# Kernel optimization log

Hardware: AMD Instinct MI355X
Metric: run time of the kernel (lower is better)

## Reference

```python
import jax, jax.numpy as jnp
import numpy as np

BN_EPS = 1e-5
SQ_EPS = 1e-12


def _mlp(x, Wa, ba, g, b, Wb, bb):
    # Linear -> BatchNorm1d (eval mode, running mean=0 var=1) -> ReLU -> Linear
    h = x @ Wa + ba
    h = h * (g / jnp.sqrt(1.0 + BN_EPS)) + b
    h = jax.nn.relu(h)
    return h @ Wb + bb


def _signed_sqrt(x):
    # sqrt(relu(x)) - sqrt(relu(-x)); tiny eps keeps grads finite at exact zeros
    return jnp.sqrt(jax.nn.relu(x) + SQ_EPS) - jnp.sqrt(jax.nn.relu(-x) + SQ_EPS)


def setup_inputs() -> dict:
    G, NPG, H, POLY, L, T, TASKS, DEG = 1024, 16, 128, 16, 3, 1048576, 1, 8
    N = G * NPG
    P = G * NPG * NPG
    E = N * DEG
    key = jax.random.key(0)
    ks = iter(jax.random.split(key, 64))

    def nrm(shape, s):
        return jax.random.normal(next(ks), shape, jnp.float32) * s

    w = 0.06  # ~xavier scale for 128-dim layers
    inp = {
        'pair_x': nrm((P, POLY), 1.0),
        'diag_x': nrm((N, POLY), 1.0),
        'node_h': nrm((N, H), 1.0),
        'edge_h': nrm((E, H), 1.0),
        'W_pair': nrm((POLY, H), 0.12),
        'W_diag': nrm((POLY, H), 0.12),
        'Wd': nrm((2 * H, TASKS), w),
        'bd': jnp.zeros((TASKS,), jnp.float32),
    }
    for p, ind in (('m1', H), ('m2', H), ('up', 2 * H)):
        inp[p + '_Wa'] = nrm((L, ind, H), w)
        inp[p + '_ba'] = jnp.zeros((L, H), jnp.float32)
        inp[p + '_g'] = jnp.ones((L, H), jnp.float32)
        inp[p + '_b'] = jnp.zeros((L, H), jnp.float32)
        inp[p + '_Wb'] = nrm((L, H, H), w)
        inp[p + '_bb'] = jnp.zeros((L, H), jnp.float32)
    inp['edge_pos'] = jax.random.randint(next(ks), (E,), 0, P)
    n = jnp.arange(N)
    inp['diag_pos'] = (n // NPG) * NPG * NPG + (n % NPG) * NPG + (n % NPG)
    # graph-local triples: base pair block of the graph + random local pair ids
    tg = jax.random.randint(next(ks), (T,), 0, G) * (NPG * NPG)
    loc = jax.random.randint(next(ks), (3, T), 0, NPG * NPG)
    inp['triple_index'] = tg[None, :] + loc
    inp['batch'] = jnp.repeat(jnp.arange(G), NPG)
    inp['pair_x_batch'] = jnp.repeat(jnp.arange(G), NPG * NPG)
    inp['ptr'] = jnp.arange(G + 1) * NPG
    inp['pair_x_ptr'] = jnp.arange(G + 1) * (NPG * NPG)
    return inp


def reference(pair_x, diag_x, node_h, edge_h, W_pair, W_diag,
              m1_Wa, m1_ba, m1_g, m1_b, m1_Wb, m1_bb,
              m2_Wa, m2_ba, m2_g, m2_b, m2_Wb, m2_bb,
              up_Wa, up_ba, up_g, up_b, up_Wb, up_bb,
              Wd, bd,
              edge_pos, diag_pos, triple_index, batch, pair_x_batch, ptr, pair_x_ptr):
    P = pair_x.shape[0]
    # InitLayer: coalesce-add of pair, edge and diagonal (node) contributions
    pair_h = pair_x @ W_pair                             # [P, H]
    pair_h = pair_h.at[edge_pos].add(edge_h)
    pair_h = pair_h.at[diag_pos].add(node_h + diag_x @ W_diag)
    idx0, idx1, idx2 = triple_index[0], triple_index[1], triple_index[2]
    L = m1_Wa.shape[0]
    for l in range(L):  # fixed small layer count
        h1 = _mlp(pair_h, m1_Wa[l], m1_ba[l], m1_g[l], m1_b[l], m1_Wb[l], m1_bb[l])
        h2 = _mlp(pair_h, m2_Wa[l], m2_ba[l], m2_g[l], m2_b[l], m2_Wb[l], m2_bb[l])
        x3 = h1[idx1] * h2[idx2]                         # [T, H] gather-multiply
        agg = jax.ops.segment_sum(x3, idx0, num_segments=P)  # scatter_add
        agg = _signed_sqrt(agg)                          # use_sqrt=True
        h = jnp.concatenate([pair_h, agg], axis=-1)      # [P, 2H]
        pair_h = _mlp(h, up_Wa[l], up_ba[l], up_g[l], up_b[l], up_Wb[l], up_bb[l]) + pair_h
    G = ptr.shape[0] - 1
    agg_all = jax.ops.segment_sum(pair_h, pair_x_batch, num_segments=G)
    agg_diag = jax.ops.segment_sum(pair_h[diag_pos], batch, num_segments=G)
    agg_off = agg_all - agg_diag
    node_sz = jnp.diff(ptr)[:, None].astype(pair_h.dtype)
    pair_sz = jnp.diff(pair_x_ptr)[:, None].astype(pair_h.dtype)
    agg_off = agg_off / jnp.maximum(pair_sz - node_sz, 1.0)  # 'mean' pooling
    agg_diag = agg_diag / node_sz
    graph_h = jnp.concatenate([agg_diag, agg_off], axis=-1)  # [G, 2H]
    return graph_h @ Wd + bd                             # output decoder
```

## Files before the change

kernel.cpp:

```cpp
#include <hip/hip_runtime.h>
#include <hip/hip_bf16.h>

#define H 128
#define POLY 16
#define PPG 256
#define GNUM 1024
#define PTOT 262144
#define NTOT 16384
#define ETOT 131072
#define TTOT 1048576

#define NCHUNK 4
#define GPC (GNUM / NCHUNK)
#define ROWS (PTOT / NCHUNK)

#define NB PTOT

#define XS 136

typedef __attribute__((ext_vector_type(8))) _Float16       f16x8;
typedef __attribute__((ext_vector_type(8))) unsigned short ushort8;
typedef __attribute__((ext_vector_type(4))) float          f32x4;

__device__ __forceinline__ unsigned short f2h(float f) {
    _Float16 h = (_Float16)f;
    return __builtin_bit_cast(unsigned short, h);
}
__device__ __forceinline__ float h2f(unsigned short u) {
    _Float16 h = __builtin_bit_cast(_Float16, u);
    return (float)h;
}
__device__ __forceinline__ void split2(float x, unsigned short& h, unsigned short& l)
{
    h = f2h(x);
    l = f2h(x - h2f(h));
}
__device__ __forceinline__ f16x8 ldf16(const unsigned short* p)
{
    return __builtin_bit_cast(f16x8, *(const ushort8*)p);
}

__global__ __launch_bounds__(256)
void k_init_pair(const float* __restrict__ px, const float* __restrict__ Wp,
                 float* __restrict__ ph)
{
    const int tid = threadIdx.x;
    const int c4 = (tid & 31) * 4;
    float4 w[POLY];
#pragma unroll
    for (int k = 0; k < POLY; ++k) w[k] = *(const float4*)(Wp + k * H + c4);
    const size_t r0 = (size_t)blockIdx.x * 64 + (tid >> 5) * 8;
#pragma unroll
    for (int rr = 0; rr < 8; ++rr) {
        const size_t p = r0 + rr;
        const float4* xp = (const float4*)(px + p * POLY);
        const float4 v0 = xp[0], v1 = xp[1], v2 = xp[2], v3 = xp[3];
        const float x[POLY] = {v0.x, v0.y, v0.z, v0.w, v1.x, v1.y, v1.z, v1.w,
                               v2.x, v2.y, v2.z, v2.w, v3.x, v3.y, v3.z, v3.w};
        float4 a = make_float4(0.f, 0.f, 0.f, 0.f);
#pragma unroll
        for (int k = 0; k < POLY; ++k) {
            a.x = fmaf(x[k], w[k].x, a.x);
            a.y = fmaf(x[k], w[k].y, a.y);
            a.z = fmaf(x[k], w[k].z, a.z);
            a.w = fmaf(x[k], w[k].w, a.w);
        }
        *(float4*)(ph + p * H + c4) = a;
    }
}

__global__ __launch_bounds__(256)
void k_edge(const float* __restrict__ eh, const int* __restrict__ epos, float* ph)
{
    const int tid = threadIdx.x;
    const size_t e = (size_t)blockIdx.x * 2 + (tid >> 7);
    const int c = tid & 127;
    atomicAdd(&ph[(size_t)epos[e] * H + c], eh[e * H + c]);
}

__global__ __launch_bounds__(256)
void k_diag(const float* __restrict__ nh, const float* __restrict__ dx,
            const float* __restrict__ Wdg, const int* __restrict__ dpos, float* ph)
{
    const int tid = threadIdx.x;
    const int c4 = (tid & 31) * 4;
    float4 w[POLY];
#pragma unroll
    for (int k = 0; k < POLY; ++k) w[k] = *(const float4*)(Wdg + k * H + c4);
    const size_t n0 = (size_t)blockIdx.x * 64 + (tid >> 5) * 8;
#pragma unroll
    for (int rr = 0; rr < 8; ++rr) {
        const size_t n = n0 + rr;
        const float4* xp = (const float4*)(dx + n * POLY);
        const float4 v0 = xp[0], v1 = xp[1], v2 = xp[2], v3 = xp[3];
        const float x[POLY] = {v0.x, v0.y, v0.z, v0.w, v1.x, v1.y, v1.z, v1.w,
                               v2.x, v2.y, v2.z, v2.w, v3.x, v3.y, v3.z, v3.w};
        const float4 nv = *(const float4*)(nh + n * H + c4);
        float4 a = nv;
#pragma unroll
        for (int k = 0; k < POLY; ++k) {
            a.x = fmaf(x[k], w[k].x, a.x);
            a.y = fmaf(x[k], w[k].y, a.y);
            a.z = fmaf(x[k], w[k].z, a.z);
            a.w = fmaf(x[k], w[k].w, a.w);
        }
        float* dst = ph + (size_t)dpos[n] * H + c4;
        const float4 old = *(const float4*)dst;
        a.x += old.x; a.y += old.y; a.z += old.z; a.w += old.w;
        *(float4*)dst = a;
    }
}

__global__ __launch_bounds__(1024)
void k_zero(int* counts) { counts[blockIdx.x * 1024 + threadIdx.x] = 0; }

__global__ __launch_bounds__(256)
void k_count(const int* __restrict__ i0, int* counts)
{
    const int t = blockIdx.x * 256 + threadIdx.x;
    atomicAdd(&counts[i0[t]], 1);
}

__global__ __launch_bounds__(1024)
void k_scan1(const int* __restrict__ counts, int* __restrict__ offs, int* __restrict__ bsum)
{
    __shared__ int s[1024];
    const int t = threadIdx.x;
    const int i = blockIdx.x * 1024 + t;
    const int v = counts[i];
    s[t] = v;
    __syncthreads();
    for (int d = 1; d < 1024; d <<= 1) {
        int add = (t >= d) ? s[t - d] : 0;
        __syncthreads();
        s[t] += add;
        __syncthreads();
    }
    offs[i] = s[t] - v;
    if (t == 1023) bsum[blockIdx.x] = s[1023];
}

__global__ __launch_bounds__(256)
void k_scan2(const int* __restrict__ bsum, int* __restrict__ bbase)
{
    __shared__ int s[256];
    const int t = threadIdx.x;
    const int v = bsum[t];
    s[t] = v;
    __syncthreads();
    for (int d = 1; d < 256; d <<= 1) {
        int add = (t >= d) ? s[t - d] : 0;
        __syncthreads();
        s[t] += add;
        __syncthreads();
    }
    bbase[t] = s[t] - v;
}

__global__ __launch_bounds__(1024)
void k_scan3(int* __restrict__ offs, const int* __restrict__ bbase, int* __restrict__ cursor)
{
    const int i = blockIdx.x * 1024 + threadIdx.x;
    const int o = offs[i] + bbase[blockIdx.x];
    offs[i] = o;
    cursor[i] = o;
    if (i == 0) offs[NB] = TTOT;
}

__global__ __launch_bounds__(256)
void k_fill(const int* __restrict__ i0, const int* __restrict__ i1,
            const int* __restrict__ i2, int* cursor, unsigned short* __restrict__ tri16)
{
    const int t = blockIdx.x * 256 + threadIdx.x;
    const int a0 = i0[t];
    const int pos = atomicAdd(&cursor[a0], 1);
    tri16[pos] = (unsigned short)((i1[t] & 255) | ((i2[t] & 255) << 8));
}

__device__ __forceinline__ void stage2(const float* __restrict__ src,
                                       unsigned short* Xh, unsigned short* Xl, int tid)
{
#pragma unroll
    for (int it = 0; it < 4; ++it) {
        const int r = (tid >> 4) + it * 16;
        const int c = (tid & 15) * 8;
        const float4 v0 = *(const float4*)(src + (size_t)r * H + c);
        const float4 v1 = *(const float4*)(src + (size_t)r * H + c + 4);
        const float x[8] = {v0.x, v0.y, v0.z, v0.w, v1.x, v1.y, v1.z, v1.w};
        ushort8 vh, vl;
#pragma unroll
        for (int j = 0; j < 8; ++j) {
            unsigned short hh, ll;
            split2(x[j], hh, ll);
            vh[j] = hh; vl[j] = ll;
        }
        *(ushort8*)(Xh + r * XS + c) = vh;
        *(ushort8*)(Xl + r * XS + c) = vl;
    }
}

#define MFMA16F(A, B, C) __builtin_amdgcn_mfma_f32_16x16x32_f16(A, B, C, 0, 0, 0)

__device__ __forceinline__ void gemm2(const unsigned short* Xh, const unsigned short* Xl,
                                      const unsigned short* __restrict__ wp,
                                      const int rt, const int cb, const int lane,
                                      f32x4 (&acc)[2][4])
{
    const int arow = lane & 15, akb = (lane >> 4) * 8;
#pragma unroll
    for (int kc = 0; kc < 4; ++kc) {
        const int kin = kc * 32 + akb;
        f16x8 ah[2], al[2];
#pragma unroll
        for (int s = 0; s < 2; ++s) {
            const int ro = (rt + s * 16 + arow) * XS + kin;
            ah[s] = ldf16(Xh + ro);
            al[s] = ldf16(Xl + ro);
        }
#pragma unroll
        for (int j = 0; j < 4; ++j) {
            const unsigned short* bp = wp + (size_t)(kc * 8 + cb + j) * 1024 + lane * 8;
            const f16x8 bh = ldf16(bp);
            const f16x8 bl = ldf16(bp + 512);
#pragma unroll
            for (int s = 0; s < 2; ++s) {
                acc[s][j] = MFMA16F(ah[s], bh, acc[s][j]);
                acc[s][j] = MFMA16F(al[s], bh, acc[s][j]);
                acc[s][j] = MFMA16F(ah[s], bl, acc[s][j]);
                acc[s][j] = MFMA16F(al[s], bl, acc[s][j]);
            }
        }
    }
}

__device__ __forceinline__ void mlp_m12_body(int bid, const float* __restrict__ x1,
    const unsigned short* __restrict__ wa1, const float* __restrict__ ba1,
    const float* __restrict__ gg1, const float* __restrict__ bsh1,
    const unsigned short* __restrict__ wb1, const float* __restrict__ bb1,
    float* __restrict__ out1,
    const unsigned short* __restrict__ wa2, const float* __restrict__ ba2,
    const float* __restrict__ gg2, const float* __restrict__ bsh2,
    const unsigned short* __restrict__ wb2, const float* __restrict__ bb2,
    float* __restrict__ out2,
    unsigned short* Xh, unsigned short* Xl, int tid)
{
    const int lane = tid & 63, wid = tid >> 6;
    const int sel = bid & 1;
    const size_t row0 = (size_t)(bid >> 1) * 64;

    const unsigned short* wa = sel ? wa2 : wa1;
    const unsigned short* wb = sel ? wb2 : wb1;
    const float* ba  = sel ? ba2  : ba1;
    const float* gg  = sel ? gg2  : gg1;
    const float* bsh = sel ? bsh2 : bsh1;
    const float* bb  = sel ? bb2  : bb1;
    float* out = sel ? out2 : out1;

    const int rt = (wid >> 1) * 32;
    const int cb = (wid & 1) * 4;

    f32x4 acc[2][4];
#pragma unroll
    for (int s = 0; s < 2; ++s)
#pragma unroll
        for (int j = 0; j < 4; ++j)
#pragma unroll
            for (int q = 0; q < 4; ++q) acc[s][j][q] = 0.f;

    stage2(x1 + row0 * H, Xh, Xl, tid);
    __syncthreads();
    gemm2(Xh, Xl, wa, rt, cb, lane, acc);
    __syncthreads();

    const float inv_s = rsqrtf(1.0f + 1e-5f);
    const int crow = (lane >> 4) * 4, ccol = lane & 15;
#pragma unroll
    for (int j = 0; j < 4; ++j) {
        const int col = (cb + j) * 16 + ccol;
        const float g  = gg[col] * inv_s;
        const float a_ = ba[col];
        const float b_ = bsh[col];
#pragma unroll
        for (int s = 0; s < 2; ++s)
#pragma unroll
            for (int q = 0; q < 4; ++q) {
                float t = fmaf(acc[s][j][q] + a_, g, b_);
                t = fmaxf(t, 0.f);
                unsigned short hh, ll;
                split2(t, hh, ll);
                const int ro = (rt + s * 16 + crow + q) * XS + col;
                Xh[ro] = hh; Xl[ro] = ll;
                acc[s][j][q] = 0.f;
            }
    }
    __syncthreads();

    gemm2(Xh, Xl, wb, rt, cb, lane, acc);

#pragma unroll
    for (int j = 0; j < 4; ++j) {
        const int col = (cb + j) * 16 + ccol;
        const float bbv = bb[col];
#pragma unroll
        for (int s = 0; s < 2; ++s)
#pragma unroll
            for (int q = 0; q < 4; ++q) {
                const int row = rt + s * 16 + crow + q;
                out[(row0 + row) * H + col] = acc[s][j][q] + bbv;
            }
    }
}

__device__ __forceinline__ void mlp_up_body(int bid, const float* __restrict__ x1,
    const float* __restrict__ x2,
    const unsigned short* __restrict__ wpa, const float* __restrict__ ba,
    const float* __restrict__ gg, const float* __restrict__ bsh,
    const unsigned short* __restrict__ wpb, const float* __restrict__ bb,
    float* __restrict__ out,
    unsigned short* Xh, unsigned short* Xl, int tid)
{
    const int lane = tid & 63, wid = tid >> 6;
    const size_t row0 = (size_t)bid * 64;
    const int rt = (wid >> 1) * 32;
    const int cb = (wid & 1) * 4;

    f32x4 acc[2][4];
#pragma unroll
    for (int s = 0; s < 2; ++s)
#pragma unroll
        for (int j = 0; j < 4; ++j)
#pragma unroll
            for (int q = 0; q < 4; ++q) acc[s][j][q] = 0.f;

    stage2(x1 + row0 * H, Xh, Xl, tid);
    __syncthreads();
    gemm2(Xh, Xl, wpa, rt, cb, lane, acc);
    __syncthreads();
    stage2(x2 + row0 * H, Xh, Xl, tid);
    __syncthreads();
    gemm2(Xh, Xl, wpa + 32 * 1024, rt, cb, lane, acc);
    __syncthreads();

    const float inv_s = rsqrtf(1.0f + 1e-5f);
    const int crow = (lane >> 4) * 4, ccol = lane & 15;
#pragma unroll
    for (int j = 0; j < 4; ++j) {
        const int col = (cb + j) * 16 + ccol;
        const float g  = gg[col] * inv_s;
        const float a_ = ba[col];
        const float b_ = bsh[col];
#pragma unroll
        for (int s = 0; s < 2; ++s)
#pragma unroll
            for (int q = 0; q < 4; ++q) {
                float t = fmaf(acc[s][j][q] + a_, g, b_);
                t = fmaxf(t, 0.f);
                unsigned short hh, ll;
                split2(t, hh, ll);
                const int ro = (rt + s * 16 + crow + q) * XS + col;
                Xh[ro] = hh; Xl[ro] = ll;
                acc[s][j][q] = 0.f;
            }
    }
    __syncthreads();

    gemm2(Xh, Xl, wpb, rt, cb, lane, acc);

#pragma unroll
    for (int j = 0; j < 4; ++j) {
        const int col = (cb + j) * 16 + ccol;
        const float bbv = bb[col];
#pragma unroll
        for (int s = 0; s < 2; ++s)
#pragma unroll
            for (int q = 0; q < 4; ++q) {
                const int row = rt + s * 16 + crow + q;
                float o = acc[s][j][q] + bbv + x1[(row0 + row) * H + col];
                out[(row0 + row) * H + col] = o;
            }
    }
}

__global__ __launch_bounds__(256)
void k_mlp_m12(const float* x1,
               const unsigned short* wa1, const float* ba1, const float* gg1,
               const float* bsh1, const unsigned short* wb1, const float* bb1, float* out1,
               const unsigned short* wa2, const float* ba2, const float* gg2,
               const float* bsh2, const unsigned short* wb2, const float* bb2, float* out2)
{
    __shared__ unsigned short Xh[64 * XS], Xl[64 * XS];
    mlp_m12_body(blockIdx.x, x1, wa1, ba1, gg1, bsh1, wb1, bb1, out1,
                 wa2, ba2, gg2, bsh2, wb2, bb2, out2, Xh, Xl, threadIdx.x);
}

__global__ __launch_bounds__(256)
void k_mlp_up(const float* x1, const float* x2,
              const unsigned short* wpa, const float* ba, const float* gg,
              const float* bsh, const unsigned short* wpb, const float* bb, float* out)
{
    __shared__ unsigned short Xh[64 * XS], Xl[64 * XS];
    mlp_up_body(blockIdx.x, x1, x2, wpa, ba, gg, bsh, wpb, bb, out,
                Xh, Xl, threadIdx.x);
}

__global__ __launch_bounds__(256)
void k_fused(const float* ux1, const float* ux2,
             const unsigned short* uwpa, const float* uba, const float* ugg,
             const float* ubsh, const unsigned short* uwpb, const float* ubb, float* uout,
             const float* mx1,
             const unsigned short* mwa1, const float* mba1, const float* mgg1,
             const float* mbsh1, const unsigned short* mwb1, const float* mbb1, float* mout1,
             const unsigned short* mwa2, const float* mba2, const float* mgg2,
             const float* mbsh2, const unsigned short* mwb2, const float* mbb2, float* mout2)
{
    __shared__ unsigned short Xh[64 * XS], Xl[64 * XS];
    const int bid = blockIdx.x;
    if (bid < ROWS / 64) {
        mlp_up_body(bid, ux1, ux2, uwpa, uba, ugg, ubsh, uwpb, ubb, uout,
                    Xh, Xl, threadIdx.x);
    } else {
        mlp_m12_body(bid - ROWS / 64, mx1, mwa1, mba1, mgg1, mbsh1, mwb1, mbb1, mout1,
                     mwa2, mba2, mgg2, mbsh2, mwb2, mbb2, mout2, Xh, Xl, threadIdx.x);
    }
}

__global__ __launch_bounds__(64)
void k_prepack2(const float* __restrict__ W, int lstride,
                unsigned short* __restrict__ outp, int ostride)
{
    const int l = blockIdx.y;
    const float* w = W + (size_t)l * lstride;
    unsigned short* o = outp + (size_t)l * ostride + (size_t)blockIdx.x * 1024;
    const int lane = threadIdx.x;
    const int kbase = (blockIdx.x >> 3) * 32 + (lane >> 4) * 8;
    const int col   = (blockIdx.x & 7) * 16 + (lane & 15);
    ushort8 vh, vl;
#pragma unroll
    for (int j = 0; j < 8; ++j) {
        unsigned short hh, ll;
        split2(w[(size_t)(kbase + j) * H + col], hh, ll);
        vh[j] = hh; vl[j] = ll;
    }
    *(ushort8*)(o + lane * 8)       = vh;
    *(ushort8*)(o + 512 + lane * 8) = vl;
}

__global__ __launch_bounds__(256)
void k_triple_s(const float* __restrict__ h1, const float* __restrict__ h2,
                const unsigned short* __restrict__ tri16,
                const int* __restrict__ offs,
                float* __restrict__ aggout)
{
    const int lane = threadIdx.x & 63;
    const int lp   = blockIdx.x * 4 + (threadIdx.x >> 6);
    const int start = offs[lp], end = offs[lp + 1];
    const size_t base = (size_t)(lp >> 8) * PPG * H + lane * 2;
    float ax = 0.f, ay = 0.f;
    unsigned us = (start < end) ? tri16[start] : 0u;
    for (int t = start; t < end; ++t) {
        const unsigned usn = (t + 1 < end) ? tri16[t + 1] : 0u;
        const float2 a = *(const float2*)&h1[base + (size_t)(us & 255u) * H];
        const float2 b = *(const float2*)&h2[base + (size_t)(us >> 8) * H];
        ax = fmaf(a.x, b.x, ax);
        ay = fmaf(a.y, b.y, ay);
        us = usn;
    }
    float2 r;
    r.x = sqrtf(fmaxf(ax, 0.f) + 1e-12f) - sqrtf(fmaxf(-ax, 0.f) + 1e-12f);
    r.y = sqrtf(fmaxf(ay, 0.f) + 1e-12f) - sqrtf(fmaxf(-ay, 0.f) + 1e-12f);
    *(float2*)&aggout[(size_t)lp * H + lane * 2] = r;
}

__global__ __launch_bounds__(256)
void k_pool(const float* __restrict__ ph, const float* __restrict__ Wd,
            const float* __restrict__ bd, float* __restrict__ out)
{
    const int g = blockIdx.x;
    const int tid = threadIdx.x;
    const int c = tid & 127, half = tid >> 7;
    const size_t base = (size_t)g * PPG * H;
    float s = 0.f;
    for (int r = half * 128; r < half * 128 + 128; ++r)
        s += ph[base + (size_t)r * H + c];
    __shared__ float sother[128];
    __shared__ float red[128];
    if (half) sother[c] = s;
    __syncthreads();
    if (!half) {
        const float tot = s + sother[c];
        float d = 0.f;
#pragma unroll
        for (int i = 0; i < 16; ++i)
            d += ph[base + (size_t)(i * 17) * H + c];
        const float diag = d * (1.f / 16.f);
        const float offv = (tot - d) * (1.f / 240.f);
        red[c] = fmaf(diag, Wd[c], offv * Wd[128 + c]);
    }
    __syncthreads();
    if (tid < 64) {
        float r = red[tid] + red[tid + 64];
#pragma unroll
        for (int off = 32; off; off >>= 1) r += __shfl_down(r, off);
        if (tid == 0) out[g] = r + bd[0];
    }
}

extern "C" void kernel_launch(void* const* d_in, const int* in_sizes, int n_in,
                              void* d_out, int out_size, void* d_ws, size_t ws_size,
                              hipStream_t stream)
{
    (void)in_sizes; (void)n_in; (void)out_size;
    const size_t OFF_PH  = 0;
    const size_t OFF_HA  = 134217728;
    const size_t OFF_HB  = 167772160;
    const size_t OFF_AGG = 201326592;
    const size_t OFF_TRI = 234881024;
    const size_t OFF_INT = 236978176;
    const size_t OFF_WP  = 240128000;
    const size_t NEED    = OFF_WP + 1376256;
    if (ws_size < NEED) return;

    const float* pair_x = (const float*)d_in[0];
    const float* diag_x = (const float*)d_in[1];
    const float* node_h = (const float*)d_in[2];
    const float* edge_h = (const float*)d_in[3];
    const float* W_pair = (const float*)d_in[4];
    const float* W_diag = (const float*)d_in[5];
    const float* Wd     = (const float*)d_in[6];
    const float* bd     = (const float*)d_in[7];
    const float* mW[3][6];
    for (int p = 0; p < 3; ++p)
        for (int q = 0; q < 6; ++q)
            mW[p][q] = (const float*)d_in[8 + p * 6 + q];
    const int* edge_pos = (const int*)d_in[26];
    const int* diag_pos = (const int*)d_in[27];
    const int* tri_idx  = (const int*)d_in[28];

    char* w = (char*)d_ws;
    float*          ph   = (float*)(w + OFF_PH);
    float*          hA   = (float*)(w + OFF_HA);
    float*          hB   = (float*)(w + OFF_HB);
    float*          aggC = (float*)(w + OFF_AGG);
    unsigned short* tri16 = (unsigned short*)(w + OFF_TRI);
    int*            counts = (int*)(w + OFF_INT);
    int*            offs   = counts + NB;
    int*            cursor = offs + NB + 8;
    int*            bsum   = cursor + NB;
    int*            bbase  = bsum + 256;
    unsigned short* wp   = (unsigned short*)(w + OFF_WP);

    const int WPL = 229376;

    k_init_pair<<<PTOT / 64, 256, 0, stream>>>(pair_x, W_pair, ph);
    k_edge<<<ETOT / 2, 256, 0, stream>>>(edge_h, edge_pos, ph);
    k_diag<<<NTOT / 64, 256, 0, stream>>>(node_h, diag_x, W_diag, diag_pos, ph);

    k_prepack2<<<dim3(32, 3), 64, 0, stream>>>(mW[0][0], 16384, wp + 0,      WPL);
    k_prepack2<<<dim3(32, 3), 64, 0, stream>>>(mW[0][4], 16384, wp + 32768,  WPL);
    k_prepack2<<<dim3(32, 3), 64, 0, stream>>>(mW[1][0], 16384, wp + 65536,  WPL);
    k_prepack2<<<dim3(32, 3), 64, 0, stream>>>(mW[1][4], 16384, wp + 98304,  WPL);
    k_prepack2<<<dim3(64, 3), 64, 0, stream>>>(mW[2][0], 32768, wp + 131072, WPL);
    k_prepack2<<<dim3(32, 3), 64, 0, stream>>>(mW[2][4], 16384, wp + 196608, WPL);

    k_zero<<<NB / 1024, 1024, 0, stream>>>(counts);
    k_count<<<TTOT / 256, 256, 0, stream>>>(tri_idx, counts);
    k_scan1<<<NB / 1024, 1024, 0, stream>>>(counts, offs, bsum);
    k_scan2<<<1, 256, 0, stream>>>(bsum, bbase);
    k_scan3<<<NB / 1024, 1024, 0, stream>>>(offs, bbase, cursor);
    k_fill<<<TTOT / 256, 256, 0, stream>>>(tri_idx, tri_idx + TTOT, tri_idx + 2 * TTOT,
                                           cursor, tri16);

    {
        const unsigned short* wl = wp;
        k_mlp_m12<<<ROWS / 64 * 2, 256, 0, stream>>>(ph,
            wl + 0,      mW[0][1], mW[0][2], mW[0][3], wl + 32768,  mW[0][5], hA,
            wl + 65536,  mW[1][1], mW[1][2], mW[1][3], wl + 98304,  mW[1][5], hB);
    }
    for (int l = 0; l < 3; ++l) {
        const unsigned short* wl = wp + (size_t)l * WPL;
        for (int c = 0; c < NCHUNK; ++c) {
            float* phc = ph + (size_t)c * ROWS * H;
            k_triple_s<<<ROWS / 4, 256, 0, stream>>>(hA, hB, tri16,
                                                     offs + (size_t)c * ROWS, aggC);
            const bool has_next = (c < NCHUNK - 1) || (l < 2);
            if (has_next) {
                const int nl = (c < NCHUNK - 1) ? l : l + 1;
                const int nc = (c < NCHUNK - 1) ? c + 1 : 0;
                const unsigned short* wn = wp + (size_t)nl * WPL;
                float* phn = ph + (size_t)nc * ROWS * H;
                k_fused<<<ROWS / 64 * 3, 256, 0, stream>>>(
                    phc, aggC,
                    wl + 131072, mW[2][1] + l * 128, mW[2][2] + l * 128,
                    mW[2][3] + l * 128, wl + 196608, mW[2][5] + l * 128, phc,
                    phn,
                    wn + 0,      mW[0][1] + nl * 128, mW[0][2] + nl * 128,
                    mW[0][3] + nl * 128, wn + 32768,  mW[0][5] + nl * 128, hA,
                    wn + 65536,  mW[1][1] + nl * 128, mW[1][2] + nl * 128,
                    mW[1][3] + nl * 128, wn + 98304,  mW[1][5] + nl * 128, hB);
            } else {
                k_mlp_up<<<ROWS / 64, 256, 0, stream>>>(phc, aggC,
                    wl + 131072, mW[2][1] + l * 128, mW[2][2] + l * 128,
                    mW[2][3] + l * 128, wl + 196608, mW[2][5] + l * 128, phc);
            }
        }
    }
    k_pool<<<GNUM, 256, 0, stream>>>(ph, Wd, bd, (float*)d_out);
}
```

Baseline: 1.695 ms.

## Software-pipeline MLP, triple-gather and update stages in one interleaved kernel

```diff
diff --git a/kernel.cpp b/kernel.cpp
--- a/kernel.cpp
+++ b/kernel.cpp
@@ -10,9 +10,10 @@
 #define ETOT 131072
 #define TTOT 1048576
 
-#define NCHUNK 4
+#define NCHUNK 8
 #define GPC (GNUM / NCHUNK)
 #define ROWS (PTOT / NCHUNK)
+#define NITER (3 * NCHUNK)
 
 #define NB PTOT
 
@@ -381,78 +382,12 @@
     }
 }
 
-__global__ __launch_bounds__(256)
-void k_mlp_m12(const float* x1,
-               const unsigned short* wa1, const float* ba1, const float* gg1,
-               const float* bsh1, const unsigned short* wb1, const float* bb1, float* out1,
-               const unsigned short* wa2, const float* ba2, const float* gg2,
-               const float* bsh2, const unsigned short* wb2, const float* bb2, float* out2)
-{
-    __shared__ unsigned short Xh[64 * XS], Xl[64 * XS];
-    mlp_m12_body(blockIdx.x, x1, wa1, ba1, gg1, bsh1, wb1, bb1, out1,
-                 wa2, ba2, gg2, bsh2, wb2, bb2, out2, Xh, Xl, threadIdx.x);
-}
-
-__global__ __launch_bounds__(256)
-void k_mlp_up(const float* x1, const float* x2,
-              const unsigned short* wpa, const float* ba, const float* gg,
-              const float* bsh, const unsigned short* wpb, const float* bb, float* out)
-{
-    __shared__ unsigned short Xh[64 * XS], Xl[64 * XS];
-    mlp_up_body(blockIdx.x, x1, x2, wpa, ba, gg, bsh, wpb, bb, out,
-                Xh, Xl, threadIdx.x);
-}
-
-__global__ __launch_bounds__(256)
-void k_fused(const float* ux1, const float* ux2,
-             const unsigned short* uwpa, const float* uba, const float* ugg,
-             const float* ubsh, const unsigned short* uwpb, const float* ubb, float* uout,
-             const float* mx1,
-             const unsigned short* mwa1, const float* mba1, const float* mgg1,
-             const float* mbsh1, const unsigned short* mwb1, const float* mbb1, float* mout1,
-             const unsigned short* mwa2, const float* mba2, const float* mgg2,
-             const float* mbsh2, const unsigned short* mwb2, const float* mbb2, float* mout2)
-{
-    __shared__ unsigned short Xh[64 * XS], Xl[64 * XS];
-    const int bid = blockIdx.x;
-    if (bid < ROWS / 64) {
-        mlp_up_body(bid, ux1, ux2, uwpa, uba, ugg, ubsh, uwpb, ubb, uout,
-                    Xh, Xl, threadIdx.x);
-    } else {
-        mlp_m12_body(bid - ROWS / 64, mx1, mwa1, mba1, mgg1, mbsh1, mwb1, mbb1, mout1,
-                     mwa2, mba2, mgg2, mbsh2, mwb2, mbb2, mout2, Xh, Xl, threadIdx.x);
-    }
-}
-
-__global__ __launch_bounds__(64)
-void k_prepack2(const float* __restrict__ W, int lstride,
-                unsigned short* __restrict__ outp, int ostride)
-{
-    const int l = blockIdx.y;
-    const float* w = W + (size_t)l * lstride;
-    unsigned short* o = outp + (size_t)l * ostride + (size_t)blockIdx.x * 1024;
-    const int lane = threadIdx.x;
-    const int kbase = (blockIdx.x >> 3) * 32 + (lane >> 4) * 8;
-    const int col   = (blockIdx.x & 7) * 16 + (lane & 15);
-    ushort8 vh, vl;
-#pragma unroll
-    for (int j = 0; j < 8; ++j) {
-        unsigned short hh, ll;
-        split2(w[(size_t)(kbase + j) * H + col], hh, ll);
-        vh[j] = hh; vl[j] = ll;
-    }
-    *(ushort8*)(o + lane * 8)       = vh;
-    *(ushort8*)(o + 512 + lane * 8) = vl;
-}
-
-__global__ __launch_bounds__(256)
-void k_triple_s(const float* __restrict__ h1, const float* __restrict__ h2,
-                const unsigned short* __restrict__ tri16,
-                const int* __restrict__ offs,
-                float* __restrict__ aggout)
-{
-    const int lane = threadIdx.x & 63;
-    const int lp   = blockIdx.x * 4 + (threadIdx.x >> 6);
+__device__ __forceinline__ void triple_body(int tb, const float* __restrict__ h1,
+    const float* __restrict__ h2, const unsigned short* __restrict__ tri16,
+    const int* __restrict__ offs, float* __restrict__ aggout, int tid)
+{
+    const int lane = tid & 63;
+    const int lp   = tb * 4 + (tid >> 6);
     const int start = offs[lp], end = offs[lp + 1];
     const size_t base = (size_t)(lp >> 8) * PPG * H + lane * 2;
     float ax = 0.f, ay = 0.f;
@@ -469,6 +404,74 @@
     r.x = sqrtf(fmaxf(ax, 0.f) + 1e-12f) - sqrtf(fmaxf(-ax, 0.f) + 1e-12f);
     r.y = sqrtf(fmaxf(ay, 0.f) + 1e-12f) - sqrtf(fmaxf(-ay, 0.f) + 1e-12f);
     *(float2*)&aggout[(size_t)lp * H + lane * 2] = r;
+}
+
+__global__ __launch_bounds__(256)
+void k_mlp_m12(const float* x1,
+               const unsigned short* wa1, const float* ba1, const float* gg1,
+               const float* bsh1, const unsigned short* wb1, const float* bb1, float* out1,
+               const unsigned short* wa2, const float* ba2, const float* gg2,
+               const float* bsh2, const unsigned short* wb2, const float* bb2, float* out2)
+{
+    __shared__ unsigned short Xh[64 * XS], Xl[64 * XS];
+    mlp_m12_body(blockIdx.x, x1, wa1, ba1, gg1, bsh1, wb1, bb1, out1,
+                 wa2, ba2, gg2, bsh2, wb2, bb2, out2, Xh, Xl, threadIdx.x);
+}
+
+__global__ __launch_bounds__(256)
+void k_pipe(int nm, int nu, int nt, int ilv,
+            const float* mx1,
+            const unsigned short* mwa1, const float* mba1, const float* mgg1,
+            const float* mbsh1, const unsigned short* mwb1, const float* mbb1, float* mout1,
+            const unsigned short* mwa2, const float* mba2, const float* mgg2,
+            const float* mbsh2, const unsigned short* mwb2, const float* mbb2, float* mout2,
+            const float* ux1, const float* ux2,
+            const unsigned short* uwpa, const float* uba, const float* ugg,
+            const float* ubsh, const unsigned short* uwpb, const float* ubb, float* uout,
+            const float* th1, const float* th2, const unsigned short* tri16,
+            const int* toffs, float* tagg)
+{
+    __shared__ unsigned short Xh[64 * XS], Xl[64 * XS];
+    const int bid = blockIdx.x, tid = threadIdx.x;
+    int type, id;
+    if (ilv) {
+        const int g = bid / 19, r = bid % 19;
+        if (r < 2)       { type = 0; id = g * 2 + r; }
+        else if (r == 2) { type = 1; id = g; }
+        else             { type = 2; id = g * 16 + (r - 3); }
+    } else {
+        if (bid < nm)            { type = 0; id = bid; }
+        else if (bid < nm + nu)  { type = 1; id = bid - nm; }
+        else                     { type = 2; id = bid - nm - nu; }
+    }
+    if (type == 0)
+        mlp_m12_body(id, mx1, mwa1, mba1, mgg1, mbsh1, mwb1, mbb1, mout1,
+                     mwa2, mba2, mgg2, mbsh2, mwb2, mbb2, mout2, Xh, Xl, tid);
+    else if (type == 1)
+        mlp_up_body(id, ux1, ux2, uwpa, uba, ugg, ubsh, uwpb, ubb, uout, Xh, Xl, tid);
+    else
+        triple_body(id, th1, th2, tri16, toffs, tagg, tid);
+}
+
+__global__ __launch_bounds__(64)
+void k_prepack2(const float* __restrict__ W, int lstride,
+                unsigned short* __restrict__ outp, int ostride)
+{
+    const int l = blockIdx.y;
+    const float* w = W + (size_t)l * lstride;
+    unsigned short* o = outp + (size_t)l * ostride + (size_t)blockIdx.x * 1024;
+    const int lane = threadIdx.x;
+    const int kbase = (blockIdx.x >> 3) * 32 + (lane >> 4) * 8;
+    const int col   = (blockIdx.x & 7) * 16 + (lane & 15);
+    ushort8 vh, vl;
+#pragma unroll
+    for (int j = 0; j < 8; ++j) {
+        unsigned short hh, ll;
+        split2(w[(size_t)(kbase + j) * H + col], hh, ll);
+        vh[j] = hh; vl[j] = ll;
+    }
+    *(ushort8*)(o + lane * 8)       = vh;
+    *(ushort8*)(o + 512 + lane * 8) = vl;
 }
 
 __global__ __launch_bounds__(256)
@@ -538,9 +541,9 @@
 
     char* w = (char*)d_ws;
     float*          ph   = (float*)(w + OFF_PH);
-    float*          hA   = (float*)(w + OFF_HA);
-    float*          hB   = (float*)(w + OFF_HB);
-    float*          aggC = (float*)(w + OFF_AGG);
+    float*          hA0  = (float*)(w + OFF_HA);
+    float*          hB0  = (float*)(w + OFF_HB);
+    float*          ag0  = (float*)(w + OFF_AGG);
     unsigned short* tri16 = (unsigned short*)(w + OFF_TRI);
     int*            counts = (int*)(w + OFF_INT);
     int*            offs   = counts + NB;
@@ -549,6 +552,10 @@
     int*            bbase  = bsum + 256;
     unsigned short* wp   = (unsigned short*)(w + OFF_WP);
 
+    float* hA[2] = {hA0, hA0 + (size_t)ROWS * H};
+    float* hB[2] = {hB0, hB0 + (size_t)ROWS * H};
+    float* ag[2] = {ag0, ag0 + (size_t)ROWS * H};
+
     const int WPL = 229376;
 
     k_init_pair<<<PTOT / 64, 256, 0, stream>>>(pair_x, W_pair, ph);
@@ -570,39 +577,42 @@
     k_fill<<<TTOT / 256, 256, 0, stream>>>(tri_idx, tri_idx + TTOT, tri_idx + 2 * TTOT,
                                            cursor, tri16);
 
-    {
-        const unsigned short* wl = wp;
-        k_mlp_m12<<<ROWS / 64 * 2, 256, 0, stream>>>(ph,
-            wl + 0,      mW[0][1], mW[0][2], mW[0][3], wl + 32768,  mW[0][5], hA,
-            wl + 65536,  mW[1][1], mW[1][2], mW[1][3], wl + 98304,  mW[1][5], hB);
-    }
-    for (int l = 0; l < 3; ++l) {
-        const unsigned short* wl = wp + (size_t)l * WPL;
-        for (int c = 0; c < NCHUNK; ++c) {
-            float* phc = ph + (size_t)c * ROWS * H;
-            k_triple_s<<<ROWS / 4, 256, 0, stream>>>(hA, hB, tri16,
-                                                     offs + (size_t)c * ROWS, aggC);
-            const bool has_next = (c < NCHUNK - 1) || (l < 2);
-            if (has_next) {
-                const int nl = (c < NCHUNK - 1) ? l : l + 1;
-                const int nc = (c < NCHUNK - 1) ? c + 1 : 0;
-                const unsigned short* wn = wp + (size_t)nl * WPL;
-                float* phn = ph + (size_t)nc * ROWS * H;
-                k_fused<<<ROWS / 64 * 3, 256, 0, stream>>>(
-                    phc, aggC,
-                    wl + 131072, mW[2][1] + l * 128, mW[2][2] + l * 128,
-                    mW[2][3] + l * 128, wl + 196608, mW[2][5] + l * 128, phc,
-                    phn,
-                    wn + 0,      mW[0][1] + nl * 128, mW[0][2] + nl * 128,
-                    mW[0][3] + nl * 128, wn + 32768,  mW[0][5] + nl * 128, hA,
-                    wn + 65536,  mW[1][1] + nl * 128, mW[1][2] + nl * 128,
-                    mW[1][3] + nl * 128, wn + 98304,  mW[1][5] + nl * 128, hB);
-            } else {
-                k_mlp_up<<<ROWS / 64, 256, 0, stream>>>(phc, aggC,
-                    wl + 131072, mW[2][1] + l * 128, mW[2][2] + l * 128,
-                    mW[2][3] + l * 128, wl + 196608, mW[2][5] + l * 128, phc);
-            }
-        }
+    const int NM = ROWS / 64 * 2;
+    const int NU = ROWS / 64;
+    const int NT = ROWS / 4;
+
+    k_mlp_m12<<<NM, 256, 0, stream>>>(ph,
+        wp + 0,     mW[0][1], mW[0][2], mW[0][3], wp + 32768, mW[0][5], hA[0],
+        wp + 65536, mW[1][1], mW[1][2], mW[1][3], wp + 98304, mW[1][5], hB[0]);
+
+    for (int i = 1; i <= NITER + 1; ++i) {
+        const int tm = i, tt = i - 1, tu = i - 2;
+        const bool hasM = (tm < NITER);
+        const bool hasT = (tt < NITER);
+        const bool hasU = (tu >= 0);
+        const int nm = hasM ? NM : 0, nu = hasU ? NU : 0, nt = hasT ? NT : 0;
+        const int ilv = (hasM && hasU && hasT) ? 1 : 0;
+
+        const int lm = hasM ? tm / NCHUNK : 0, cm = hasM ? tm % NCHUNK : 0;
+        const int lu = hasU ? tu / NCHUNK : 0, cu = hasU ? tu % NCHUNK : 0;
+        const int ct = hasT ? tt % NCHUNK : 0;
+
+        const unsigned short* wm = wp + (size_t)lm * WPL;
+        const unsigned short* wu = wp + (size_t)lu * WPL;
+        const float* phm = ph + (size_t)cm * ROWS * H;
+        float*       phu = ph + (size_t)cu * ROWS * H;
+
+        k_pipe<<<nm + nu + nt, 256, 0, stream>>>(nm, nu, nt, ilv,
+            phm,
+            wm + 0,     mW[0][1] + lm * 128, mW[0][2] + lm * 128, mW[0][3] + lm * 128,
+            wm + 32768, mW[0][5] + lm * 128, hA[tm & 1],
+            wm + 65536, mW[1][1] + lm * 128, mW[1][2] + lm * 128, mW[1][3] + lm * 128,
+            wm + 98304, mW[1][5] + lm * 128, hB[tm & 1],
+            phu, ag[tu >= 0 ? (tu & 1) : 0],
+            wu + 131072, mW[2][1] + lu * 128, mW[2][2] + lu * 128, mW[2][3] + lu * 128,
+            wu + 196608, mW[2][5] + lu * 128, phu,
+            hA[tt >= 0 ? (tt & 1) : 0], hB[tt >= 0 ? (tt & 1) : 0], tri16,
+            offs + (size_t)ct * ROWS, ag[tt >= 0 ? (tt & 1) : 0]);
     }
     k_pool<<<GNUM, 256, 0, stream>>>(ph, Wd, bd, (float*)d_out);
 }
```

Result: slower. 2.210 ms (+30.4%).

## Merge prologue kernels into block-partitioned launches to cut launch count

Applied to the files above, without the earlier changes.

```diff
diff --git a/kernel.cpp b/kernel.cpp
--- a/kernel.cpp
+++ b/kernel.cpp
@@ -40,16 +40,15 @@
     return __builtin_bit_cast(f16x8, *(const ushort8*)p);
 }
 
-__global__ __launch_bounds__(256)
-void k_init_pair(const float* __restrict__ px, const float* __restrict__ Wp,
-                 float* __restrict__ ph)
-{
-    const int tid = threadIdx.x;
+__device__ __forceinline__ void init_pair_body(int bid, const float* __restrict__ px,
+                                               const float* __restrict__ Wp,
+                                               float* __restrict__ ph, int tid)
+{
     const int c4 = (tid & 31) * 4;
     float4 w[POLY];
 #pragma unroll
     for (int k = 0; k < POLY; ++k) w[k] = *(const float4*)(Wp + k * H + c4);
-    const size_t r0 = (size_t)blockIdx.x * 64 + (tid >> 5) * 8;
+    const size_t r0 = (size_t)bid * 64 + (tid >> 5) * 8;
 #pragma unroll
     for (int rr = 0; rr < 8; ++rr) {
         const size_t p = r0 + rr;
@@ -69,57 +68,100 @@
     }
 }
 
-__global__ __launch_bounds__(256)
-void k_edge(const float* __restrict__ eh, const int* __restrict__ epos, float* ph)
-{
-    const int tid = threadIdx.x;
-    const size_t e = (size_t)blockIdx.x * 2 + (tid >> 7);
-    const int c = tid & 127;
-    atomicAdd(&ph[(size_t)epos[e] * H + c], eh[e * H + c]);
-}
-
-__global__ __launch_bounds__(256)
-void k_diag(const float* __restrict__ nh, const float* __restrict__ dx,
-            const float* __restrict__ Wdg, const int* __restrict__ dpos, float* ph)
-{
-    const int tid = threadIdx.x;
-    const int c4 = (tid & 31) * 4;
-    float4 w[POLY];
-#pragma unroll
-    for (int k = 0; k < POLY; ++k) w[k] = *(const float4*)(Wdg + k * H + c4);
-    const size_t n0 = (size_t)blockIdx.x * 64 + (tid >> 5) * 8;
-#pragma unroll
-    for (int rr = 0; rr < 8; ++rr) {
-        const size_t n = n0 + rr;
-        const float4* xp = (const float4*)(dx + n * POLY);
-        const float4 v0 = xp[0], v1 = xp[1], v2 = xp[2], v3 = xp[3];
-        const float x[POLY] = {v0.x, v0.y, v0.z, v0.w, v1.x, v1.y, v1.z, v1.w,
-                               v2.x, v2.y, v2.z, v2.w, v3.x, v3.y, v3.z, v3.w};
-        const float4 nv = *(const float4*)(nh + n * H + c4);
-        float4 a = nv;
-#pragma unroll
-        for (int k = 0; k < POLY; ++k) {
-            a.x = fmaf(x[k], w[k].x, a.x);
-            a.y = fmaf(x[k], w[k].y, a.y);
-            a.z = fmaf(x[k], w[k].z, a.z);
-            a.w = fmaf(x[k], w[k].w, a.w);
+__device__ __forceinline__ void prepack_body(const float* __restrict__ W,
+                                             unsigned short* __restrict__ o_base,
+                                             int b, int lane)
+{
+    unsigned short* o = o_base + (size_t)b * 1024;
+    const int kbase = (b >> 3) * 32 + (lane >> 4) * 8;
+    const int col   = (b & 7) * 16 + (lane & 15);
+    ushort8 vh, vl;
+#pragma unroll
+    for (int j = 0; j < 8; ++j) {
+        unsigned short hh, ll;
+        split2(W[(size_t)(kbase + j) * H + col], hh, ll);
+        vh[j] = hh; vl[j] = ll;
+    }
+    *(ushort8*)(o + lane * 8)       = vh;
+    *(ushort8*)(o + 512 + lane * 8) = vl;
+}
+
+#define WPL 229376
+
+__global__ __launch_bounds__(256)
+void k_prologue(const float* __restrict__ px, const float* __restrict__ Wp,
+                float* __restrict__ ph,
+                const int* __restrict__ i0, int* __restrict__ counts,
+                const float* __restrict__ Wm1a, const float* __restrict__ Wm1b,
+                const float* __restrict__ Wm2a, const float* __restrict__ Wm2b,
+                const float* __restrict__ Wupa, const float* __restrict__ Wupb,
+                unsigned short* __restrict__ wp)
+{
+    const int bid = blockIdx.x, tid = threadIdx.x;
+    if (bid < 4096) {
+        init_pair_body(bid, px, Wp, ph, tid);
+    } else if (bid < 8192) {
+        const int t = (bid - 4096) * 256 + tid;
+        atomicAdd(&counts[i0[t]], 1);
+    } else {
+        const int f = (bid - 8192) * 4 + (tid >> 6);
+        const int lane = tid & 63;
+        const int layer = f / 224, r = f % 224;
+        unsigned short* wl = wp + (size_t)layer * WPL;
+        if (r < 32)       prepack_body(Wm1a + (size_t)layer * 16384, wl + 0,      r,       lane);
+        else if (r < 64)  prepack_body(Wm1b + (size_t)layer * 16384, wl + 32768,  r - 32,  lane);
+        else if (r < 96)  prepack_body(Wm2a + (size_t)layer * 16384, wl + 65536,  r - 64,  lane);
+        else if (r < 128) prepack_body(Wm2b + (size_t)layer * 16384, wl + 98304,  r - 96,  lane);
+        else if (r < 192) prepack_body(Wupa + (size_t)layer * 32768, wl + 131072, r - 128, lane);
+        else              prepack_body(Wupb + (size_t)layer * 16384, wl + 196608, r - 192, lane);
+    }
+}
+
+__global__ __launch_bounds__(256)
+void k_edgediag(const float* __restrict__ eh, const int* __restrict__ epos,
+                const float* __restrict__ nh, const float* __restrict__ dx,
+                const float* __restrict__ Wdg, const int* __restrict__ dpos,
+                float* ph)
+{
+    const int bid = blockIdx.x, tid = threadIdx.x;
+    if (bid < ETOT / 2) {
+        const size_t e = (size_t)bid * 2 + (tid >> 7);
+        const int c = tid & 127;
+        atomicAdd(&ph[(size_t)epos[e] * H + c], eh[e * H + c]);
+    } else {
+        const int db = bid - ETOT / 2;
+        const int c4 = (tid & 31) * 4;
+        float4 w[POLY];
+#pragma unroll
+        for (int k = 0; k < POLY; ++k) w[k] = *(const float4*)(Wdg + k * H + c4);
+        const size_t n0 = (size_t)db * 64 + (tid >> 5) * 8;
+#pragma unroll
+        for (int rr = 0; rr < 8; ++rr) {
+            const size_t n = n0 + rr;
+            const float4* xp = (const float4*)(dx + n * POLY);
+            const float4 v0 = xp[0], v1 = xp[1], v2 = xp[2], v3 = xp[3];
+            const float x[POLY] = {v0.x, v0.y, v0.z, v0.w, v1.x, v1.y, v1.z, v1.w,
+                                   v2.x, v2.y, v2.z, v2.w, v3.x, v3.y, v3.z, v3.w};
+            const float4 nv = *(const float4*)(nh + n * H + c4);
+            float4 a = nv;
+#pragma unroll
+            for (int k = 0; k < POLY; ++k) {
+                a.x = fmaf(x[k], w[k].x, a.x);
+                a.y = fmaf(x[k], w[k].y, a.y);
+                a.z = fmaf(x[k], w[k].z, a.z);
+                a.w = fmaf(x[k], w[k].w, a.w);
+            }
+            float* dst = ph + (size_t)dpos[n] * H + c4;
+            atomicAdd(dst + 0, a.x);
+            atomicAdd(dst + 1, a.y);
+            atomicAdd(dst + 2, a.z);
+            atomicAdd(dst + 3, a.w);
         }
-        float* dst = ph + (size_t)dpos[n] * H + c4;
-        const float4 old = *(const float4*)dst;
-        a.x += old.x; a.y += old.y; a.z += old.z; a.w += old.w;
-        *(float4*)dst = a;
     }
 }
 
 __global__ __launch_bounds__(1024)
 void k_zero(int* counts) { counts[blockIdx.x * 1024 + threadIdx.x] = 0; }
-
-__global__ __launch_bounds__(256)
-void k_count(const int* __restrict__ i0, int* counts)
-{
-    const int t = blockIdx.x * 256 + threadIdx.x;
-    atomicAdd(&counts[i0[t]], 1);
-}
 
 __global__ __launch_bounds__(1024)
 void k_scan1(const int* __restrict__ counts, int* __restrict__ offs, int* __restrict__ bsum)
@@ -165,16 +207,6 @@
     offs[i] = o;
     cursor[i] = o;
     if (i == 0) offs[NB] = TTOT;
-}
-
-__global__ __launch_bounds__(256)
-void k_fill(const int* __restrict__ i0, const int* __restrict__ i1,
-            const int* __restrict__ i2, int* cursor, unsigned short* __restrict__ tri16)
-{
-    const int t = blockIdx.x * 256 + threadIdx.x;
-    const int a0 = i0[t];
-    const int pos = atomicAdd(&cursor[a0], 1);
-    tri16[pos] = (unsigned short)((i1[t] & 255) | ((i2[t] & 255) << 8));
 }
 
 __device__ __forceinline__ void stage2(const float* __restrict__ src,
@@ -382,15 +414,26 @@
 }
 
 __global__ __launch_bounds__(256)
-void k_mlp_m12(const float* x1,
+void k_m12fill(const float* x1,
                const unsigned short* wa1, const float* ba1, const float* gg1,
                const float* bsh1, const unsigned short* wb1, const float* bb1, float* out1,
                const unsigned short* wa2, const float* ba2, const float* gg2,
-               const float* bsh2, const unsigned short* wb2, const float* bb2, float* out2)
+               const float* bsh2, const unsigned short* wb2, const float* bb2, float* out2,
+               const int* __restrict__ i0, const int* __restrict__ i1,
+               const int* __restrict__ i2, int* cursor,
+               unsigned short* __restrict__ tri16)
 {
     __shared__ unsigned short Xh[64 * XS], Xl[64 * XS];
-    mlp_m12_body(blockIdx.x, x1, wa1, ba1, gg1, bsh1, wb1, bb1, out1,
-                 wa2, ba2, gg2, bsh2, wb2, bb2, out2, Xh, Xl, threadIdx.x);
+    const int bid = blockIdx.x, tid = threadIdx.x;
+    if (bid < ROWS / 64 * 2) {
+        mlp_m12_body(bid, x1, wa1, ba1, gg1, bsh1, wb1, bb1, out1,
+                     wa2, ba2, gg2, bsh2, wb2, bb2, out2, Xh, Xl, tid);
+    } else {
+        const int t = (bid - ROWS / 64 * 2) * 256 + tid;
+        const int a0 = i0[t];
+        const int pos = atomicAdd(&cursor[a0], 1);
+        tri16[pos] = (unsigned short)((i1[t] & 255) | ((i2[t] & 255) << 8));
+    }
 }
 
 __global__ __launch_bounds__(256)
@@ -422,27 +465,6 @@
         mlp_m12_body(bid - ROWS / 64, mx1, mwa1, mba1, mgg1, mbsh1, mwb1, mbb1, mout1,
                      mwa2, mba2, mgg2, mbsh2, mwb2, mbb2, mout2, Xh, Xl, threadIdx.x);
     }
-}
-
-__global__ __launch_bounds__(64)
-void k_prepack2(const float* __restrict__ W, int lstride,
-                unsigned short* __restrict__ outp, int ostride)
-{
-    const int l = blockIdx.y;
-    const float* w = W + (size_t)l * lstride;
-    unsigned short* o = outp + (size_t)l * ostride + (size_t)blockIdx.x * 1024;
-    const int lane = threadIdx.x;
-    const int kbase = (blockIdx.x >> 3) * 32 + (lane >> 4) * 8;
-    const int col   = (blockIdx.x & 7) * 16 + (lane & 15);
-    ushort8 vh, vl;
-#pragma unroll
-    for (int j = 0; j < 8; ++j) {
-        unsigned short hh, ll;
-        split2(w[(size_t)(kbase + j) * H + col], hh, ll);
-        vh[j] = hh; vl[j] = ll;
-    }
-    *(ushort8*)(o + lane * 8)       = vh;
-    *(ushort8*)(o + 512 + lane * 8) = vl;
 }
 
 __global__ __launch_bounds__(256)
@@ -549,33 +571,23 @@
     int*            bbase  = bsum + 256;
     unsigned short* wp   = (unsigned short*)(w + OFF_WP);
 
-    const int WPL = 229376;
-
-    k_init_pair<<<PTOT / 64, 256, 0, stream>>>(pair_x, W_pair, ph);
-    k_edge<<<ETOT / 2, 256, 0, stream>>>(edge_h, edge_pos, ph);
-    k_diag<<<NTOT / 64, 256, 0, stream>>>(node_h, diag_x, W_diag, diag_pos, ph);
-
-    k_prepack2<<<dim3(32, 3), 64, 0, stream>>>(mW[0][0], 16384, wp + 0,      WPL);
-    k_prepack2<<<dim3(32, 3), 64, 0, stream>>>(mW[0][4], 16384, wp + 32768,  WPL);
-    k_prepack2<<<dim3(32, 3), 64, 0, stream>>>(mW[1][0], 16384, wp + 65536,  WPL);
-    k_prepack2<<<dim3(32, 3), 64, 0, stream>>>(mW[1][4], 16384, wp + 98304,  WPL);
-    k_prepack2<<<dim3(64, 3), 64, 0, stream>>>(mW[2][0], 32768, wp + 131072, WPL);
-    k_prepack2<<<dim3(32, 3), 64, 0, stream>>>(mW[2][4], 16384, wp + 196608, WPL);
 
     k_zero<<<NB / 1024, 1024, 0, stream>>>(counts);
-    k_count<<<TTOT / 256, 256, 0, stream>>>(tri_idx, counts);
+    k_prologue<<<4096 + 4096 + 168, 256, 0, stream>>>(pair_x, W_pair, ph,
+        tri_idx, counts,
+        mW[0][0], mW[0][4], mW[1][0], mW[1][4], mW[2][0], mW[2][4], wp);
+    k_edgediag<<<ETOT / 2 + NTOT / 64, 256, 0, stream>>>(edge_h, edge_pos,
+        node_h, diag_x, W_diag, diag_pos, ph);
+
     k_scan1<<<NB / 1024, 1024, 0, stream>>>(counts, offs, bsum);
     k_scan2<<<1, 256, 0, stream>>>(bsum, bbase);
     k_scan3<<<NB / 1024, 1024, 0, stream>>>(offs, bbase, cursor);
-    k_fill<<<TTOT / 256, 256, 0, stream>>>(tri_idx, tri_idx + TTOT, tri_idx + 2 * TTOT,
-                                           cursor, tri16);
-
-    {
-        const unsigned short* wl = wp;
-        k_mlp_m12<<<ROWS / 64 * 2, 256, 0, stream>>>(ph,
-            wl + 0,      mW[0][1], mW[0][2], mW[0][3], wl + 32768,  mW[0][5], hA,
-            wl + 65536,  mW[1][1], mW[1][2], mW[1][3], wl + 98304,  mW[1][5], hB);
-    }
+
+    k_m12fill<<<ROWS / 64 * 2 + TTOT / 256, 256, 0, stream>>>(ph,
+        wp + 0,     mW[0][1], mW[0][2], mW[0][3], wp + 32768, mW[0][5], hA,
+        wp + 65536, mW[1][1], mW[1][2], mW[1][3], wp + 98304, mW[1][5], hB,
+        tri_idx, tri_idx + TTOT, tri_idx + 2 * TTOT, cursor, tri16);
+
     for (int l = 0; l < 3; ++l) {
         const unsigned short* wl = wp + (size_t)l * WPL;
         for (int c = 0; c < NCHUNK; ++c) {
```

Result: slower. 1.738 ms (+2.6%).
